# Performance work log

Hardware: AMD Instinct MI355X
Metric: run time of the kernel (lower is better)

Reference implementation:

```python
import jax, jax.numpy as jnp
import numpy as np

BH, N, C, T = 16, 2048, 64, 64


def setup_inputs() -> dict:
    key = jax.random.key(0)
    k1, k2, k3 = jax.random.split(key, 3)
    q = jax.random.normal(k1, (BH, N, C), dtype=jnp.float32)
    qk = jax.random.normal(k2, (BH, N, N), dtype=jnp.float32)
    # learned positional embedding (1, C, T); random instead of zeros so the
    # gather/interpolation path is numerically non-trivial
    pos_emb = jax.random.normal(k3, (1, C, T), dtype=jnp.float32)
    return {"q": q, "qk": qk, "pos_emb": pos_emb}


def reference(q, qk, pos_emb):
    T_ = pos_emb.shape[-1]
    # gate: g_ij = sigmoid(q_i . k_j)
    G = jax.nn.sigmoid(qk)                                   # (BH, N, N)
    # reverse cumulative sum along last dim: p_ij = sum_{k=j..N-1} g_ik
    P = jnp.flip(jnp.cumsum(jnp.flip(G, axis=-1), axis=-1), axis=-1)
    P = jnp.minimum(P, T_ - 1)                                # clamp(max=T-1)
    P_ceil = jnp.ceil(P).astype(jnp.int32)                    # (BH, N, N)
    P_floor = jnp.floor(P).astype(jnp.int32)
    # E[b, n, t] = q[b, n, :] @ pos_emb[0, :, t]  -> (BH, N, T)
    E = jnp.einsum('bnc,ct->bnt', q, pos_emb[0])
    E_ceil = jnp.take_along_axis(E, P_ceil, axis=-1)          # (BH, N, N)
    E_floor = jnp.take_along_axis(E, P_floor, axis=-1)
    w = P - P_floor
    return w * E_ceil + (1.0 - w) * E_floor
```

## Files before the change

kernel.cpp:

```cpp
#include <hip/hip_runtime.h>

#define BHN (16 * 2048)
#define NN  2048
#define CC  64
#define TT  64

__global__ __launch_bounds__(256, 4) void cope_kernel(
    const float* __restrict__ q,
    const float* __restrict__ qk,
    const float* __restrict__ pos_emb,
    float* __restrict__ out)
{
    const int row  = blockIdx.x;
    const int tid  = threadIdx.x;
    const int lane = tid & 63;
    const int wv   = tid >> 6;

    __shared__ float q_lds[CC];
    __shared__ float e_part[4][TT];
    __shared__ float e_row[TT];
    __shared__ float wave_tot[4];

    const size_t rowN = (size_t)row * NN;

    const float4* qk4 = (const float4*)(qk + rowN);
    float4 v0 = qk4[tid * 2];
    float4 v1 = qk4[tid * 2 + 1];

    if (tid < CC) q_lds[tid] = q[(size_t)row * CC + tid];
    __syncthreads();

    {
        const int t  = tid & 63;
        const int c0 = (tid >> 6) * 16;
        float acc = 0.0f;
#pragma unroll
        for (int cc = 0; cc < 16; ++cc)
            acc = fmaf(q_lds[c0 + cc], pos_emb[(c0 + cc) * TT + t], acc);
        e_part[tid >> 6][t] = acc;
    }
    __syncthreads();
    if (tid < TT)
        e_row[tid] = e_part[0][tid] + e_part[1][tid] + e_part[2][tid] + e_part[3][tid];

    float g[8];
    g[0] = v0.x; g[1] = v0.y; g[2] = v0.z; g[3] = v0.w;
    g[4] = v1.x; g[5] = v1.y; g[6] = v1.z; g[7] = v1.w;
#pragma unroll
    for (int k = 0; k < 8; ++k)
        g[k] = 1.0f / (1.0f + __expf(-g[k]));

    float s = 0.0f;
#pragma unroll
    for (int k = 0; k < 8; ++k) s += g[k];

    float inc = s;
#pragma unroll
    for (int o = 1; o < 64; o <<= 1) {
        float tmp = __shfl_down(inc, o, 64);
        if (lane + o < 64) inc += tmp;
    }
    const float X = inc - s;
    if (lane == 0) wave_tot[wv] = inc;
    __syncthreads();

    float W = 0.0f;
#pragma unroll
    for (int w2 = 0; w2 < 4; ++w2)
        if (w2 > wv) W += wave_tot[w2];
    const float base = X + W;

    float o8[8];
    float run = 0.0f;
#pragma unroll
    for (int k = 7; k >= 0; --k) {
        run += g[k];
        float P  = fminf(run + base, 63.0f);
        float fl = floorf(P);
        float w_ = P - fl;
        int   i0 = (int)fl;
        int   i1 = (int)ceilf(P);
        float ef = e_row[i0];
        float ec = e_row[i1];
        o8[k] = fmaf(w_, ec - ef, ef);
    }

    float4* out4 = (float4*)(out + rowN);
    out4[tid * 2]     = make_float4(o8[0], o8[1], o8[2], o8[3]);
    out4[tid * 2 + 1] = make_float4(o8[4], o8[5], o8[6], o8[7]);
}

extern "C" void kernel_launch(void* const* d_in, const int* in_sizes, int n_in,
                              void* d_out, int out_size, void* d_ws, size_t ws_size,
                              hipStream_t stream) {
    const float* q       = (const float*)d_in[0];
    const float* qk      = (const float*)d_in[1];
    const float* pos_emb = (const float*)d_in[2];
    float* out = (float*)d_out;

    dim3 grid(BHN);
    dim3 block(256);
    cope_kernel<<<grid, block, 0, stream>>>(q, qk, pos_emb, out);
}
```

Baseline: 105.2 us.

## Process four rows per block with per-wave E computation and one barrier

Result: slower. 113.1 us (+7.5%).

```diff
diff --git a/kernel.cpp b/kernel.cpp
--- a/kernel.cpp
+++ b/kernel.cpp
@@ -1,9 +1,10 @@
 #include <hip/hip_runtime.h>
 
-#define BHN (16 * 2048)
-#define NN  2048
-#define CC  64
-#define TT  64
+#define NN   2048
+#define CC   64
+#define TT   64
+#define ROWS 4
+#define BHN  (16 * 2048)
 
 __global__ __launch_bounds__(256, 4) void cope_kernel(
     const float* __restrict__ q,
@@ -11,83 +12,91 @@
     const float* __restrict__ pos_emb,
     float* __restrict__ out)
 {
-    const int row  = blockIdx.x;
     const int tid  = threadIdx.x;
     const int lane = tid & 63;
     const int wv   = tid >> 6;
+    const int row0 = blockIdx.x * ROWS;
 
-    __shared__ float q_lds[CC];
-    __shared__ float e_part[4][TT];
-    __shared__ float e_row[TT];
-    __shared__ float wave_tot[4];
+    __shared__ float e_row[ROWS][TT];
+    __shared__ float wave_tot[ROWS][4];
 
-    const size_t rowN = (size_t)row * NN;
+    float4 v[2 * ROWS];
+#pragma unroll
+    for (int r = 0; r < ROWS; ++r) {
+        const float4* qk4 = (const float4*)(qk + (size_t)(row0 + r) * NN);
+        v[2 * r]     = qk4[2 * tid];
+        v[2 * r + 1] = qk4[2 * tid + 1];
+    }
 
-    const float4* qk4 = (const float4*)(qk + rowN);
-    float4 v0 = qk4[tid * 2];
-    float4 v1 = qk4[tid * 2 + 1];
+    {
+        const int erow = __builtin_amdgcn_readfirstlane(row0 + wv);
+        const float* qr = q + (size_t)erow * CC;
+        float acc0 = 0.0f, acc1 = 0.0f;
+#pragma unroll 8
+        for (int c = 0; c < CC; c += 2) {
+            acc0 = fmaf(qr[c],     pos_emb[c * TT + lane],       acc0);
+            acc1 = fmaf(qr[c + 1], pos_emb[(c + 1) * TT + lane], acc1);
+        }
+        e_row[wv][lane] = acc0 + acc1;
+    }
 
-    if (tid < CC) q_lds[tid] = q[(size_t)row * CC + tid];
+    float g[8 * ROWS];
+#pragma unroll
+    for (int r = 0; r < ROWS; ++r) {
+        g[8 * r + 0] = v[2 * r].x;     g[8 * r + 1] = v[2 * r].y;
+        g[8 * r + 2] = v[2 * r].z;     g[8 * r + 3] = v[2 * r].w;
+        g[8 * r + 4] = v[2 * r + 1].x; g[8 * r + 5] = v[2 * r + 1].y;
+        g[8 * r + 6] = v[2 * r + 1].z; g[8 * r + 7] = v[2 * r + 1].w;
+    }
+#pragma unroll
+    for (int k = 0; k < 8 * ROWS; ++k)
+        g[k] = __builtin_amdgcn_rcpf(1.0f + __expf(-g[k]));
+
+    float X[ROWS];
+#pragma unroll
+    for (int r = 0; r < ROWS; ++r) {
+        float s = 0.0f;
+#pragma unroll
+        for (int k = 0; k < 8; ++k) s += g[8 * r + k];
+        float inc = s;
+#pragma unroll
+        for (int o = 1; o < 64; o <<= 1) {
+            float tmp = __shfl_down(inc, o, 64);
+            if (lane + o < 64) inc += tmp;
+        }
+        X[r] = inc - s;
+        if (lane == 0) wave_tot[r][wv] = inc;
+    }
+
     __syncthreads();
 
-    {
-        const int t  = tid & 63;
-        const int c0 = (tid >> 6) * 16;
-        float acc = 0.0f;
 #pragma unroll
-        for (int cc = 0; cc < 16; ++cc)
-            acc = fmaf(q_lds[c0 + cc], pos_emb[(c0 + cc) * TT + t], acc);
-        e_part[tid >> 6][t] = acc;
+    for (int r = 0; r < ROWS; ++r) {
+        float W = 0.0f;
+#pragma unroll
+        for (int w2 = 0; w2 < 4; ++w2)
+            if (w2 > wv) W += wave_tot[r][w2];
+        const float base = X[r] + W;
+
+        float o8[8];
+        float run = 0.0f;
+#pragma unroll
+        for (int k = 7; k >= 0; --k) {
+            run += g[8 * r + k];
+            float P  = fminf(run + base, 63.0f);
+            float fl = floorf(P);
+            float w_ = P - fl;
+            int   i0 = (int)fl;
+            int   i1 = (int)ceilf(P);
+            float ef = e_row[r][i0];
+            float ec = e_row[r][i1];
+            o8[k] = fmaf(w_, ec - ef, ef);
+        }
+
+        float4* out4 = (float4*)(out + (size_t)(row0 + r) * NN);
+        out4[2 * tid]     = make_float4(o8[0], o8[1], o8[2], o8[3]);
+        out4[2 * tid + 1] = make_float4(o8[4], o8[5], o8[6], o8[7]);
     }
-    __syncthreads();
-    if (tid < TT)
-        e_row[tid] = e_part[0][tid] + e_part[1][tid] + e_part[2][tid] + e_part[3][tid];
-
-    float g[8];
-    g[0] = v0.x; g[1] = v0.y; g[2] = v0.z; g[3] = v0.w;
-    g[4] = v1.x; g[5] = v1.y; g[6] = v1.z; g[7] = v1.w;
-#pragma unroll
-    for (int k = 0; k < 8; ++k)
-        g[k] = 1.0f / (1.0f + __expf(-g[k]));
-
-    float s = 0.0f;
-#pragma unroll
-    for (int k = 0; k < 8; ++k) s += g[k];
-
-    float inc = s;
-#pragma unroll
-    for (int o = 1; o < 64; o <<= 1) {
-        float tmp = __shfl_down(inc, o, 64);
-        if (lane + o < 64) inc += tmp;
-    }
-    const float X = inc - s;
-    if (lane == 0) wave_tot[wv] = inc;
-    __syncthreads();
-
-    float W = 0.0f;
-#pragma unroll
-    for (int w2 = 0; w2 < 4; ++w2)
-        if (w2 > wv) W += wave_tot[w2];
-    const float base = X + W;
-
-    float o8[8];
-    float run = 0.0f;
-#pragma unroll
-    for (int k = 7; k >= 0; --k) {
-        run += g[k];
-        float P  = fminf(run + base, 63.0f);
-        float fl = floorf(P);
-        float w_ = P - fl;
-        int   i0 = (int)fl;
-        int   i1 = (int)ceilf(P);
-        float ef = e_row[i0];
-        float ec = e_row[i1];
-        o8[k] = fmaf(w_, ec - ef, ef);
-    }
-
-    float4* out4 = (float4*)(out + rowN);
-    out4[tid * 2]     = make_float4(o8[0], o8[1], o8[2], o8[3]);
-    out4[tid * 2 + 1] = make_float4(o8[4], o8[5], o8[6], o8[7]);
 }
 
 extern "C" void kernel_launch(void* const* d_in, const int* in_sizes, int n_in,
@@ -98,7 +107,7 @@
     const float* pos_emb = (const float*)d_in[2];
     float* out = (float*)d_out;
 
-    dim3 grid(BHN);
+    dim3 grid(BHN / ROWS);
     dim3 block(256);
     cope_kernel<<<grid, block, 0, stream>>>(q, qk, pos_emb, out);
 }
```

## Use persistent blocks with prefetched qk rows and shuffle-based E lookup

Applied to the files above, without the earlier changes.

Result: slower. 124.4 us (+18.3%).

```diff
diff --git a/kernel.cpp b/kernel.cpp
--- a/kernel.cpp
+++ b/kernel.cpp
@@ -1,9 +1,11 @@
 #include <hip/hip_runtime.h>
 
-#define BHN (16 * 2048)
-#define NN  2048
-#define CC  64
-#define TT  64
+#define NN    2048
+#define CC    64
+#define TT    64
+#define GRID  2048
+#define ITERS 16
+#define NROWS (16 * 2048)
 
 __global__ __launch_bounds__(256, 4) void cope_kernel(
     const float* __restrict__ q,
@@ -11,83 +13,97 @@
     const float* __restrict__ pos_emb,
     float* __restrict__ out)
 {
-    const int row  = blockIdx.x;
     const int tid  = threadIdx.x;
     const int lane = tid & 63;
     const int wv   = tid >> 6;
 
-    __shared__ float q_lds[CC];
-    __shared__ float e_part[4][TT];
-    __shared__ float e_row[TT];
-    __shared__ float wave_tot[4];
+    __shared__ float pe[CC * TT];
+    __shared__ float wave_tot[2][4];
 
-    const size_t rowN = (size_t)row * NN;
+    {
+        const float4* src = (const float4*)pos_emb;
+        float4* dst = (float4*)pe;
+#pragma unroll
+        for (int i = 0; i < (CC * TT / 4) / 256; ++i)
+            dst[tid + i * 256] = src[tid + i * 256];
+    }
 
-    const float4* qk4 = (const float4*)(qk + rowN);
-    float4 v0 = qk4[tid * 2];
-    float4 v1 = qk4[tid * 2 + 1];
+    int row = blockIdx.x;
+    const float4* qkp = (const float4*)(qk + (size_t)row * NN);
+    float4 a0 = qkp[2 * tid];
+    float4 a1 = qkp[2 * tid + 1];
 
-    if (tid < CC) q_lds[tid] = q[(size_t)row * CC + tid];
     __syncthreads();
 
-    {
-        const int t  = tid & 63;
-        const int c0 = (tid >> 6) * 16;
-        float acc = 0.0f;
+    for (int it = 0; it < ITERS; ++it) {
+        float4 b0 = a0, b1 = a1;
+        if (it + 1 < ITERS) {
+            const float4* np = (const float4*)(qk + (size_t)(row + GRID) * NN);
+            b0 = np[2 * tid];
+            b1 = np[2 * tid + 1];
+        }
+
+        float e;
+        {
+            const float* qr = q + (size_t)row * CC;
+            float acc0 = 0.0f, acc1 = 0.0f;
+#pragma unroll 8
+            for (int c = 0; c < CC; c += 2) {
+                acc0 = fmaf(qr[c],     pe[c * TT + lane],       acc0);
+                acc1 = fmaf(qr[c + 1], pe[(c + 1) * TT + lane], acc1);
+            }
+            e = acc0 + acc1;
+        }
+
+        float g[8];
+        g[0] = a0.x; g[1] = a0.y; g[2] = a0.z; g[3] = a0.w;
+        g[4] = a1.x; g[5] = a1.y; g[6] = a1.z; g[7] = a1.w;
 #pragma unroll
-        for (int cc = 0; cc < 16; ++cc)
-            acc = fmaf(q_lds[c0 + cc], pos_emb[(c0 + cc) * TT + t], acc);
-        e_part[tid >> 6][t] = acc;
+        for (int k = 0; k < 8; ++k)
+            g[k] = __builtin_amdgcn_rcpf(1.0f + __expf(-g[k]));
+
+        float s = 0.0f;
+#pragma unroll
+        for (int k = 0; k < 8; ++k) s += g[k];
+
+        float inc = s;
+#pragma unroll
+        for (int o = 1; o < 64; o <<= 1) {
+            float t = __shfl_down(inc, o, 64);
+            if (lane + o < 64) inc += t;
+        }
+        const float X = inc - s;
+        if (lane == 0) wave_tot[it & 1][wv] = inc;
+        __syncthreads();
+
+        float W = 0.0f;
+#pragma unroll
+        for (int w2 = 0; w2 < 4; ++w2)
+            if (w2 > wv) W += wave_tot[it & 1][w2];
+        const float base = X + W;
+
+        float o8[8];
+        float run = 0.0f;
+#pragma unroll
+        for (int k = 7; k >= 0; --k) {
+            run += g[k];
+            float P  = fminf(run + base, 63.0f);
+            float fl = floorf(P);
+            float w_ = P - fl;
+            int   i0 = (int)fl;
+            int   i1 = min(i0 + 1, 63);
+            float ef = __shfl(e, i0, 64);
+            float ec = __shfl(e, i1, 64);
+            o8[k] = fmaf(w_, ec - ef, ef);
+        }
+
+        float4* op = (float4*)(out + (size_t)row * NN);
+        op[2 * tid]     = make_float4(o8[0], o8[1], o8[2], o8[3]);
+        op[2 * tid + 1] = make_float4(o8[4], o8[5], o8[6], o8[7]);
+
+        a0 = b0; a1 = b1;
+        row += GRID;
     }
-    __syncthreads();
-    if (tid < TT)
-        e_row[tid] = e_part[0][tid] + e_part[1][tid] + e_part[2][tid] + e_part[3][tid];
-
-    float g[8];
-    g[0] = v0.x; g[1] = v0.y; g[2] = v0.z; g[3] = v0.w;
-    g[4] = v1.x; g[5] = v1.y; g[6] = v1.z; g[7] = v1.w;
-#pragma unroll
-    for (int k = 0; k < 8; ++k)
-        g[k] = 1.0f / (1.0f + __expf(-g[k]));
-
-    float s = 0.0f;
-#pragma unroll
-    for (int k = 0; k < 8; ++k) s += g[k];
-
-    float inc = s;
-#pragma unroll
-    for (int o = 1; o < 64; o <<= 1) {
-        float tmp = __shfl_down(inc, o, 64);
-        if (lane + o < 64) inc += tmp;
-    }
-    const float X = inc - s;
-    if (lane == 0) wave_tot[wv] = inc;
-    __syncthreads();
-
-    float W = 0.0f;
-#pragma unroll
-    for (int w2 = 0; w2 < 4; ++w2)
-        if (w2 > wv) W += wave_tot[w2];
-    const float base = X + W;
-
-    float o8[8];
-    float run = 0.0f;
-#pragma unroll
-    for (int k = 7; k >= 0; --k) {
-        run += g[k];
-        float P  = fminf(run + base, 63.0f);
-        float fl = floorf(P);
-        float w_ = P - fl;
-        int   i0 = (int)fl;
-        int   i1 = (int)ceilf(P);
-        float ef = e_row[i0];
-        float ec = e_row[i1];
-        o8[k] = fmaf(w_, ec - ef, ef);
-    }
-
-    float4* out4 = (float4*)(out + rowN);
-    out4[tid * 2]     = make_float4(o8[0], o8[1], o8[2], o8[3]);
-    out4[tid * 2 + 1] = make_float4(o8[4], o8[5], o8[6], o8[7]);
 }
 
 extern "C" void kernel_launch(void* const* d_in, const int* in_sizes, int n_in,
@@ -98,7 +114,7 @@
     const float* pos_emb = (const float*)d_in[2];
     float* out = (float*)d_out;
 
-    dim3 grid(BHN);
+    dim3 grid(GRID);
     dim3 block(256);
     cope_kernel<<<grid, block, 0, stream>>>(q, qk, pos_emb, out);
 }
```

## Split E projection into a separate kernel and simplify per-row interpolation kernel

Applied to the files above, without the earlier changes.

Result: slower. 120.1 us (+14.2%).

```diff
diff --git a/kernel.cpp b/kernel.cpp
--- a/kernel.cpp
+++ b/kernel.cpp
@@ -1,20 +1,118 @@
 #include <hip/hip_runtime.h>
 
-#define BHN (16 * 2048)
-#define NN  2048
-#define CC  64
-#define TT  64
-
-__global__ __launch_bounds__(256, 4) void cope_kernel(
+#define NN 2048
+#define CC 64
+#define TT 64
+#define NROWS (16 * 2048)
+
+__global__ __launch_bounds__(256, 4) void e_kernel(
+    const float* __restrict__ q,
+    const float* __restrict__ pos_emb,
+    float* __restrict__ E)
+{
+    const int lane = threadIdx.x & 63;
+    const int wv   = threadIdx.x >> 6;
+    const int row  = blockIdx.x * 4 + wv;
+    const int urow = __builtin_amdgcn_readfirstlane(row);
+    const float* qr = q + (size_t)urow * CC;
+    const float* pe = pos_emb + lane;
+    float acc0 = 0.f, acc1 = 0.f, acc2 = 0.f, acc3 = 0.f;
+#pragma unroll
+    for (int c = 0; c < CC; c += 4) {
+        acc0 = fmaf(qr[c + 0], pe[(c + 0) * TT], acc0);
+        acc1 = fmaf(qr[c + 1], pe[(c + 1) * TT], acc1);
+        acc2 = fmaf(qr[c + 2], pe[(c + 2) * TT], acc2);
+        acc3 = fmaf(qr[c + 3], pe[(c + 3) * TT], acc3);
+    }
+    E[(size_t)urow * TT + lane] = (acc0 + acc1) + (acc2 + acc3);
+}
+
+__global__ __launch_bounds__(256, 8) void cope_kernel(
+    const float* __restrict__ qk,
+    const float* __restrict__ E,
+    float* __restrict__ out)
+{
+    const int tid  = threadIdx.x;
+    const int lane = tid & 63;
+    const int wv   = tid >> 6;
+    const int row  = blockIdx.x;
+
+    __shared__ float e_lds[TT];
+    __shared__ float wave_tot[4];
+
+    const float4* qk4 = (const float4*)(qk + (size_t)row * NN);
+    float4 a0 = qk4[2 * tid];
+    float4 a1 = qk4[2 * tid + 1];
+
+    if (tid < 16)
+        ((float4*)e_lds)[tid] = ((const float4*)(E + (size_t)row * TT))[tid];
+
+    float g[8];
+    g[0] = a0.x; g[1] = a0.y; g[2] = a0.z; g[3] = a0.w;
+    g[4] = a1.x; g[5] = a1.y; g[6] = a1.z; g[7] = a1.w;
+    float s = 0.f;
+#pragma unroll
+    for (int k = 0; k < 8; ++k) {
+        g[k] = __builtin_amdgcn_rcpf(1.0f + __expf(-g[k]));
+        s += g[k];
+    }
+
+    float inc = s;
+#pragma unroll
+    for (int o = 1; o < 64; o <<= 1) {
+        float t = __shfl_down(inc, o, 64);
+        if (lane + o < 64) inc += t;
+    }
+    const float X = inc - s;
+    if (lane == 0) wave_tot[wv] = inc;
+
+    __syncthreads();
+
+    float W = 0.f;
+#pragma unroll
+    for (int w2 = 0; w2 < 4; ++w2)
+        if (w2 > wv) W += wave_tot[w2];
+    const float base = X + W;
+
+    float4 o0, o1;
+    if (base >= 63.0f) {
+        const float e63 = e_lds[63];
+        o0 = make_float4(e63, e63, e63, e63);
+        o1 = o0;
+    } else {
+        float o8[8];
+        float run = 0.f;
+#pragma unroll
+        for (int k = 7; k >= 0; --k) {
+            run += g[k];
+            float P  = fminf(run + base, 63.0f);
+            float fl = floorf(P);
+            float w  = P - fl;
+            int   i0 = (int)fl;
+            int   i1 = min(i0 + 1, 63);
+            float ef = e_lds[i0];
+            float ec = e_lds[i1];
+            o8[k] = fmaf(w, ec - ef, ef);
+        }
+        o0 = make_float4(o8[0], o8[1], o8[2], o8[3]);
+        o1 = make_float4(o8[4], o8[5], o8[6], o8[7]);
+    }
+
+    float4* op = (float4*)(out + (size_t)row * NN);
+    op[2 * tid]     = o0;
+    op[2 * tid + 1] = o1;
+}
+
+__global__ __launch_bounds__(256, 4) void cope_fused(
     const float* __restrict__ q,
     const float* __restrict__ qk,
     const float* __restrict__ pos_emb,
     float* __restrict__ out)
 {
-    const int row  = blockIdx.x;
     const int tid  = threadIdx.x;
     const int lane = tid & 63;
     const int wv   = tid >> 6;
+    const int row  = blockIdx.x;
 
     __shared__ float q_lds[CC];
     __shared__ float e_part[4][TT];
@@ -22,14 +120,12 @@
     __shared__ float wave_tot[4];
 
     const size_t rowN = (size_t)row * NN;
-
     const float4* qk4 = (const float4*)(qk + rowN);
     float4 v0 = qk4[tid * 2];
     float4 v1 = qk4[tid * 2 + 1];
 
     if (tid < CC) q_lds[tid] = q[(size_t)row * CC + tid];
     __syncthreads();
-
     {
         const int t  = tid & 63;
         const int c0 = (tid >> 6) * 16;
@@ -98,7 +194,12 @@
     const float* pos_emb = (const float*)d_in[2];
     float* out = (float*)d_out;
 
-    dim3 grid(BHN);
-    dim3 block(256);
-    cope_kernel<<<grid, block, 0, stream>>>(q, qk, pos_emb, out);
-}
+    const size_t e_bytes = (size_t)NROWS * TT * sizeof(float);
+    if (ws_size >= e_bytes) {
+        float* E = (float*)d_ws;
+        e_kernel<<<dim3(NROWS / 4), dim3(256), 0, stream>>>(q, pos_emb, E);
+        cope_kernel<<<dim3(NROWS), dim3(256), 0, stream>>>(qk, E, out);
+    } else {
+        cope_fused<<<dim3(NROWS), dim3(256), 0, stream>>>(q, qk, pos_emb, out);
+    }
+}
```
